# Optimization experiments

Hardware: AMD Instinct MI355X
Metric: run time of the kernel (lower is better)

The kernel has to match this reference:

```python
import jax, jax.numpy as jnp
import numpy as np

D_MODEL = 2048
HQ = 32
HK = 8
DK = D_MODEL // HQ  # 64
G = HQ // HK        # 4
VOCAB = 32000
B, S = 1, 2048


def setup_inputs() -> dict:
    key = jax.random.key(0)
    ks = jax.random.split(key, 7)
    scale = 1.0 / np.sqrt(D_MODEL)
    X = jax.random.randint(ks[0], (B, S), 0, VOCAB, dtype=jnp.int64)
    emb = jax.random.normal(ks[1], (VOCAB, D_MODEL), dtype=jnp.float32)
    Wk = jax.random.normal(ks[2], (HK * DK, D_MODEL), dtype=jnp.float32) * scale
    Wv = jax.random.normal(ks[3], (HK * DK, D_MODEL), dtype=jnp.float32) * scale
    Wq = jax.random.normal(ks[4], (D_MODEL, D_MODEL), dtype=jnp.float32) * scale
    Wo_w = jax.random.normal(ks[5], (D_MODEL, D_MODEL), dtype=jnp.float32) * scale
    Wo_b = jax.random.normal(ks[6], (D_MODEL,), dtype=jnp.float32) * scale
    return {"X": X, "emb": emb, "Wk": Wk, "Wv": Wv, "Wq": Wq, "Wo_w": Wo_w, "Wo_b": Wo_b}


def reference(X, emb, Wk, Wv, Wq, Wo_w, Wo_b):
    e = emb[X]  # [B,S,D]
    b, s, _ = e.shape
    # torch Linear: y = x @ W.T (weights stored [out,in])
    k = (e @ Wk.T).reshape(b, s, HK, DK)            # [B,S,Hk,dk]
    v = (e @ Wv.T).reshape(b, s, HK, DK)            # [B,S,Hk,dk]
    q = (e @ Wq.T).reshape(b, s, HK, G, DK)         # q head index = i*G + g
    # scores: [B,Hk,G,S,S] — same math as expanding KV to Hq heads, no copy
    scores = jnp.einsum('bsigd,btid->bigst', q, k) / jnp.sqrt(jnp.asarray(DK, e.dtype))
    w = jax.nn.softmax(scores, axis=-1)
    ctx = jnp.einsum('bigst,btid->bsigd', w, v).reshape(b, s, D_MODEL)
    return ctx @ Wo_w.T + Wo_b
```

## Files before the change

### kernel.cpp

```cpp
#include <hip/hip_runtime.h>


typedef __bf16 bf16x8 __attribute__((ext_vector_type(8)));
typedef float f32x4 __attribute__((ext_vector_type(4)));
typedef float f32x16 __attribute__((ext_vector_type(16)));
typedef unsigned short ushort8_t __attribute__((ext_vector_type(8)));
typedef unsigned int uint4_t __attribute__((ext_vector_type(4)));

#define DEVI static __device__ __forceinline__

#define QSCALE 0.180336880111112f

DEVI unsigned short f2bf(float f) {
    union { float f; unsigned int u; } c; c.f = f;
    unsigned int u = c.u;
    unsigned int r = (u + 0x7FFFu + ((u >> 16) & 1u)) >> 16;
    return (unsigned short)r;
}

DEVI f32x4 mfma16(bf16x8 a, bf16x8 b, f32x4 c) {
    return __builtin_amdgcn_mfma_f32_16x16x32_bf16(a, b, c, 0, 0, 0);
}
DEVI f32x16 mfma32(bf16x8 a, bf16x8 b, f32x16 c) {
    return __builtin_amdgcn_mfma_f32_32x32x16_bf16(a, b, c, 0, 0, 0);
}
DEVI unsigned cvtpk(float a, float b) {
    unsigned r;
    asm("v_cvt_pk_bf16_f32 %0, %1, %2" : "=v"(r) : "v"(a), "v"(b));
    return r;
}
DEVI void plswap(unsigned& a, unsigned& b) {
    asm("v_permlane32_swap_b32 %0, %1" : "+v"(a), "+v"(b));
}
DEVI void gload16(const unsigned short* g, unsigned short* l) {
    __builtin_amdgcn_global_load_lds(
        (const __attribute__((address_space(1))) void*)g,
        (__attribute__((address_space(3))) void*)l, 16, 0, 0);
}
#define WAIT_VM(n) asm volatile("s_waitcnt vmcnt(" #n ")" ::: "memory")
#define WAIT_LGKM0() asm volatile("s_waitcnt lgkmcnt(0)" ::: "memory")
#define BAR() __builtin_amdgcn_s_barrier()

DEVI void cvt8(const float* src, unsigned short* dst) {
    float4 f0 = *(const float4*)(src);
    float4 f1 = *(const float4*)(src + 4);
    ushort8_t v;
    v[0] = f2bf(f0.x); v[1] = f2bf(f0.y); v[2] = f2bf(f0.z); v[3] = f2bf(f0.w);
    v[4] = f2bf(f1.x); v[5] = f2bf(f1.y); v[6] = f2bf(f1.z); v[7] = f2bf(f1.w);
    *(ushort8_t*)(dst) = v;
}

__global__ __launch_bounds__(256)
void prep_k(const int* __restrict__ X, const float* __restrict__ emb,
            unsigned short* __restrict__ e,
            const float* __restrict__ Wk, unsigned short* __restrict__ Wkb,
            const float* __restrict__ Wv, unsigned short* __restrict__ Wvb,
            const float* __restrict__ Wq, unsigned short* __restrict__ Wqb,
            const float* __restrict__ Wo, unsigned short* __restrict__ Wob) {
    int b = blockIdx.x;
    if (b < 2048) {
        long long row = X[b];
        cvt8(emb + row * 2048 + threadIdx.x * 8, e + (size_t)b * 2048 + threadIdx.x * 8);
        return;
    }
    b -= 2048;
    const float* s; unsigned short* d; int off;
    if (b < 512) { s = Wk; d = Wkb; off = b; }
    else if (b < 1024) { s = Wv; d = Wvb; off = b - 512; }
    else if (b < 3072) { s = Wq; d = Wqb; off = b - 1024; }
    else { s = Wo; d = Wob; off = b - 3072; }
    size_t idx = ((size_t)off * 256 + threadIdx.x) * 8;
    cvt8(s + idx, d + idx);
}

template<int OM0, int OM1, int OM2>
__global__ __launch_bounds__(256)
void gemm_swz_k(const unsigned short* __restrict__ A,
                const unsigned short* __restrict__ W0, const unsigned short* __restrict__ W1,
                const unsigned short* __restrict__ W2,
                void* __restrict__ C0, void* __restrict__ C1, void* __restrict__ C2,
                int t1, int t2, int ldc0, int ldc1, int ldc2,
                const float* __restrict__ bias) {
    __shared__ unsigned short As[2 * 128 * 64];
    __shared__ unsigned short Bs[2 * 128 * 64];
    const int cpx = gridDim.x >> 3;
    int id = blockIdx.x;
    int swz = (id & 7) * cpx + (id >> 3);
    const int bx = swz & 15;
    const int by = swz >> 4;
    const unsigned short* Wp; void* Cp; int ldc, om, nb;
    if (by < t1)      { Wp = W0; Cp = C0; ldc = ldc0; om = OM0; nb = by; }
    else if (by < t2) { Wp = W1; Cp = C1; ldc = ldc1; om = OM1; nb = by - t1; }
    else              { Wp = W2; Cp = C2; ldc = ldc2; om = OM2; nb = by - t2; }
    const int m0 = bx * 128, n0 = nb * 128;
    const int tid = threadIdx.x, lane = tid & 63, w = tid >> 6;
    const int wm = (w >> 1) * 64, wn = (w & 1) * 64;
    const int lr = lane & 15, lg = lane >> 4;
    const int srow = tid >> 3, sj = tid & 7;

    f32x4 acc[4][4];
    #pragma unroll
    for (int i = 0; i < 4; i++)
        #pragma unroll
        for (int j = 0; j < 4; j++) acc[i][j] = {};

    #define G_STAGE(buf, k0)                                                          \
        _Pragma("unroll")                                                             \
        for (int i = 0; i < 4; i++) {                                                 \
            int row = srow + i * 32;                                                  \
            int jj = sj ^ (row & 7);                                                  \
            unsigned short* ad = As + (buf) * 8192 + (w * 64 + i * 256) * 8;          \
            unsigned short* bd = Bs + (buf) * 8192 + (w * 64 + i * 256) * 8;          \
            gload16(A  + (size_t)(m0 + row) * 2048 + (k0) + jj * 8, ad);              \
            gload16(Wp + (size_t)(n0 + row) * 2048 + (k0) + jj * 8, bd);              \
        }

    G_STAGE(0, 0);
    for (int s = 0; s < 32; ++s) {
        const int cur = s & 1;
        if (s < 31) {
            G_STAGE(cur ^ 1, (s + 1) * 64);
            WAIT_VM(8);
        } else {
            WAIT_VM(0);
        }
        BAR();
        const unsigned short* Asb = As + cur * 8192;
        const unsigned short* Bsb = Bs + cur * 8192;
        #pragma unroll
        for (int kk = 0; kk < 2; kk++) {
            bf16x8 af[4], bfr[4];
            #pragma unroll
            for (int mi = 0; mi < 4; mi++) {
                int r = wm + mi * 16 + lr;
                int g = (kk * 4 + lg) ^ (r & 7);
                af[mi] = *(const bf16x8*)(&Asb[r * 64 + g * 8]);
            }
            #pragma unroll
            for (int ni = 0; ni < 4; ni++) {
                int r = wn + ni * 16 + lr;
                int g = (kk * 4 + lg) ^ (r & 7);
                bfr[ni] = *(const bf16x8*)(&Bsb[r * 64 + g * 8]);
            }
            __builtin_amdgcn_s_setprio(1);
            #pragma unroll
            for (int mi = 0; mi < 4; mi++)
                #pragma unroll
                for (int ni = 0; ni < 4; ni++)
                    acc[mi][ni] = mfma16(af[mi], bfr[ni], acc[mi][ni]);
            __builtin_amdgcn_s_setprio(0);
        }
        WAIT_LGKM0();
        BAR();
    }
    #undef G_STAGE

    #pragma unroll
    for (int mi = 0; mi < 4; mi++)
        #pragma unroll
        for (int ni = 0; ni < 4; ni++) {
            int col = n0 + wn + ni * 16 + lr;
            #pragma unroll
            for (int jj = 0; jj < 4; jj++) {
                int rowg = m0 + wm + mi * 16 + lg * 4 + jj;
                float vv = acc[mi][ni][jj];
                if (om == 0) {
                    ((unsigned short*)Cp)[(size_t)rowg * ldc + col] = f2bf(vv);
                } else if (om == 1) {
                    ((float*)Cp)[(size_t)rowg * ldc + col] = vv + bias[col];
                } else if (om == 2) {
                    ((unsigned short*)Cp)[(size_t)col * ldc + rowg] = f2bf(vv);
                } else {
                    ((unsigned short*)Cp)[(size_t)rowg * ldc + col] = f2bf(vv * QSCALE);
                }
            }
        }
}

__global__ __launch_bounds__(256)
void attn2_k(const unsigned short* __restrict__ Qb, const unsigned short* __restrict__ Kb,
             const unsigned short* __restrict__ VbT, unsigned short* __restrict__ Ctx) {
    __shared__ unsigned short Ks[2 * 64 * 64];
    __shared__ unsigned short Vts[2 * 64 * 64];
    int id = blockIdx.x;
    int swz = (id & 7) * 64 + (id >> 3);
    const int hq = swz >> 4;
    const int qt = swz & 15;
    const int ikv = hq >> 2;
    const int tid = threadIdx.x, lane = tid & 63, w = tid >> 6;
    const int l31 = lane & 31, hi = lane >> 5;
    const int qrow = qt * 128 + w * 32 + l31;
    const int srow = tid >> 3, sj = tid & 7;

    bf16x8 qf[4];
    #pragma unroll
    for (int ks = 0; ks < 4; ks++)
        qf[ks] = *(const bf16x8*)(Qb + (size_t)qrow * 2048 + hq * 64 + ks * 16 + hi * 8);

    bf16x8 onesb;
    #pragma unroll
    for (int i = 0; i < 8; i++) onesb[i] = (__bf16)1.0f;

    f32x16 oacc0 = {}, oacc1 = {}, lacc = {};
    float m = -1e30f;

    #define A_STAGE(buf, t0)                                                          \
        _Pragma("unroll")                                                             \
        for (int i = 0; i < 2; i++) {                                                 \
            int row = srow + i * 32;                                                  \
            int jj = sj ^ (row & 7);                                                  \
            unsigned short* kd = Ks + (buf) * 4096 + (w * 64 + i * 256) * 8;          \
            unsigned short* vd = Vts + (buf) * 4096 + (w * 64 + i * 256) * 8;         \
            gload16(Kb + (size_t)((t0) + row) * 512 + ikv * 64 + jj * 8, kd);         \
            gload16(VbT + (size_t)(ikv * 64 + row) * 2048 + (t0) + jj * 8, vd);       \
        }

    A_STAGE(0, 0);
    for (int t = 0; t < 32; ++t) {
        const int cur = t & 1;
        if (t < 31) {
            A_STAGE(cur ^ 1, (t + 1) * 64);
            WAIT_VM(4);
        } else {
            WAIT_VM(0);
        }
        BAR();
        const unsigned short* Ksb = Ks + cur * 4096;
        const unsigned short* Vsb = Vts + cur * 4096;

        f32x16 s0 = {}, s1 = {};
        __builtin_amdgcn_s_setprio(1);
        #pragma unroll
        for (int ks = 0; ks < 4; ks++) {
            int gr = (2 * ks + hi) ^ (l31 & 7);
            bf16x8 kf0 = *(const bf16x8*)(&Ksb[l31 * 64 + gr * 8]);
            bf16x8 kf1 = *(const bf16x8*)(&Ksb[(32 + l31) * 64 + gr * 8]);
            s0 = mfma32(kf0, qf[ks], s0);
            s1 = mfma32(kf1, qf[ks], s1);
        }
        __builtin_amdgcn_s_setprio(0);

        float a0 = fmaxf(fmaxf(s0[0],  s0[1]),  s0[2]);
        float a1 = fmaxf(fmaxf(s0[3],  s0[4]),  s0[5]);
        float a2 = fmaxf(fmaxf(s0[6],  s0[7]),  s0[8]);
        float a3 = fmaxf(fmaxf(s0[9],  s0[10]), s0[11]);
        float a4 = fmaxf(fmaxf(s0[12], s0[13]), s0[14]);
        float b0 = fmaxf(fmaxf(s1[0],  s1[1]),  s1[2]);
        float b1 = fmaxf(fmaxf(s1[3],  s1[4]),  s1[5]);
        float b2 = fmaxf(fmaxf(s1[6],  s1[7]),  s1[8]);
        float b3 = fmaxf(fmaxf(s1[9],  s1[10]), s1[11]);
        float b4 = fmaxf(fmaxf(s1[12], s1[13]), s1[14]);
        float c0 = fmaxf(s0[15], s1[15]);
        float d0 = fmaxf(fmaxf(a0, a1), a2);
        float d1 = fmaxf(fmaxf(a3, a4), b0);
        float d2 = fmaxf(fmaxf(b1, b2), b3);
        float d3 = fmaxf(fmaxf(b4, c0), d0);
        float pmax = fmaxf(fmaxf(d1, d2), d3);
        pmax = fmaxf(pmax, __shfl_xor(pmax, 32, 64));

        if (!__all(pmax <= m + 8.0f)) {
            float mnew = fmaxf(m, pmax);
            float sc = exp2f(m - mnew);
            m = mnew;
            #pragma unroll
            for (int r = 0; r < 16; r++) {
                const int qp = (r & 3) + 8 * (r >> 2);
                float scv = __shfl(sc, qp + 4 * hi, 64);
                oacc0[r] *= scv;
                oacc1[r] *= scv;
                lacc[r] *= scv;
            }
        }

        #pragma unroll
        for (int r = 0; r < 16; r++) {
            s0[r] = exp2f(s0[r] - m);
            s1[r] = exp2f(s1[r] - m);
        }

        uint4_t pw[4];
        #pragma unroll
        for (int c = 0; c < 2; c++) {
            unsigned a   = cvtpk(s0[8 * c + 0], s0[8 * c + 1]);
            unsigned bb  = cvtpk(s0[8 * c + 2], s0[8 * c + 3]);
            unsigned cc2 = cvtpk(s0[8 * c + 4], s0[8 * c + 5]);
            unsigned dd  = cvtpk(s0[8 * c + 6], s0[8 * c + 7]);
            plswap(a, cc2); plswap(bb, dd);
            pw[c][0] = a; pw[c][1] = bb; pw[c][2] = cc2; pw[c][3] = dd;
        }
        #pragma unroll
        for (int c = 0; c < 2; c++) {
            unsigned a   = cvtpk(s1[8 * c + 0], s1[8 * c + 1]);
            unsigned bb  = cvtpk(s1[8 * c + 2], s1[8 * c + 3]);
            unsigned cc2 = cvtpk(s1[8 * c + 4], s1[8 * c + 5]);
            unsigned dd  = cvtpk(s1[8 * c + 6], s1[8 * c + 7]);
            plswap(a, cc2); plswap(bb, dd);
            pw[2 + c][0] = a; pw[2 + c][1] = bb; pw[2 + c][2] = cc2; pw[2 + c][3] = dd;
        }

        __builtin_amdgcn_s_setprio(1);
        #pragma unroll
        for (int ks = 0; ks < 4; ks++) {
            bf16x8 pa = __builtin_bit_cast(bf16x8, pw[ks]);
            int gr = (2 * ks + hi) ^ (l31 & 7);
            bf16x8 vf0 = *(const bf16x8*)(&Vsb[l31 * 64 + gr * 8]);
            bf16x8 vf1 = *(const bf16x8*)(&Vsb[(32 + l31) * 64 + gr * 8]);
            oacc0 = mfma32(pa, vf0, oacc0);
            oacc1 = mfma32(pa, vf1, oacc1);
            lacc  = mfma32(pa, onesb, lacc);
        }
        __builtin_amdgcn_s_setprio(0);
        WAIT_LGKM0();
        BAR();
    }
    #undef A_STAGE

    #pragma unroll
    for (int r = 0; r < 16; r++) {
        float lv = 1.0f / lacc[r];
        int row = qt * 128 + w * 32 + (r & 3) + 8 * (r >> 2) + 4 * hi;
        Ctx[(size_t)row * 2048 + hq * 64 + l31]      = f2bf(oacc0[r] * lv);
        Ctx[(size_t)row * 2048 + hq * 64 + 32 + l31] = f2bf(oacc1[r] * lv);
    }
}

extern "C" void kernel_launch(void* const* d_in, const int* in_sizes, int n_in,
                              void* d_out, int out_size, void* d_ws, size_t ws_size,
                              hipStream_t stream) {
    (void)in_sizes; (void)n_in; (void)out_size; (void)ws_size;
    const int*   X   = (const int*)d_in[0];
    const float* emb = (const float*)d_in[1];
    const float* Wk  = (const float*)d_in[2];
    const float* Wv  = (const float*)d_in[3];
    const float* Wq  = (const float*)d_in[4];
    const float* Wo  = (const float*)d_in[5];
    const float* Wb  = (const float*)d_in[6];

    unsigned short* e   = (unsigned short*)d_ws;
    unsigned short* Kb  = e   + (size_t)2048 * 2048;
    unsigned short* VbT = Kb  + (size_t)2048 * 512;
    unsigned short* Qb  = VbT + (size_t)512 * 2048;
    unsigned short* Ctx = Qb  + (size_t)2048 * 2048;
    unsigned short* Wkb = Ctx + (size_t)2048 * 2048;
    unsigned short* Wvb = Wkb + (size_t)512 * 2048;
    unsigned short* Wqb = Wvb + (size_t)512 * 2048;
    unsigned short* Wob = Wqb + (size_t)2048 * 2048;

    prep_k<<<dim3(2048 + 5120), dim3(256), 0, stream>>>(X, emb, e, Wk, Wkb, Wv, Wvb,
                                                        Wq, Wqb, Wo, Wob);
    gemm_swz_k<3, 0, 2><<<dim3(384), dim3(256), 0, stream>>>(
        e, Wqb, Wkb, Wvb, (void*)Qb, (void*)Kb, (void*)VbT,
        16, 20, 2048, 512, 2048, nullptr);
    attn2_k<<<dim3(512), dim3(256), 0, stream>>>(Qb, Kb, VbT, Ctx);
    gemm_swz_k<1, 1, 1><<<dim3(256), dim3(256), 0, stream>>>(
        Ctx, Wob, Wob, Wob, d_out, d_out, d_out,
        16, 32, 2048, 2048, 2048, Wb);
}
```

Measured before the change: 162.9 us.

## Load K/V fragments directly from global memory into registers in attention

```diff
diff --git a/kernel.cpp b/kernel.cpp
--- a/kernel.cpp
+++ b/kernel.cpp
@@ -178,19 +178,16 @@
 }
 
 __global__ __launch_bounds__(256)
-void attn2_k(const unsigned short* __restrict__ Qb, const unsigned short* __restrict__ Kb,
+void attn3_k(const unsigned short* __restrict__ Qb, const unsigned short* __restrict__ Kb,
              const unsigned short* __restrict__ VbT, unsigned short* __restrict__ Ctx) {
-    __shared__ unsigned short Ks[2 * 64 * 64];
-    __shared__ unsigned short Vts[2 * 64 * 64];
     int id = blockIdx.x;
     int swz = (id & 7) * 64 + (id >> 3);
     const int hq = swz >> 4;
     const int qt = swz & 15;
     const int ikv = hq >> 2;
-    const int tid = threadIdx.x, lane = tid & 63, w = tid >> 6;
+    const int lane = threadIdx.x & 63, w = threadIdx.x >> 6;
     const int l31 = lane & 31, hi = lane >> 5;
     const int qrow = qt * 128 + w * 32 + l31;
-    const int srow = tid >> 3, sj = tid & 7;
 
     bf16x8 qf[4];
     #pragma unroll
@@ -201,42 +198,33 @@
     #pragma unroll
     for (int i = 0; i < 8; i++) onesb[i] = (__bf16)1.0f;
 
+    const unsigned short* Kp0 = Kb + (size_t)l31 * 512 + ikv * 64 + hi * 8;
+    const unsigned short* Kp1 = Kp0 + (size_t)32 * 512;
+    const unsigned short* Vp0 = VbT + (size_t)(ikv * 64 + l31) * 2048 + hi * 8;
+    const unsigned short* Vp1 = Vp0 + (size_t)32 * 2048;
+
     f32x16 oacc0 = {}, oacc1 = {}, lacc = {};
     float m = -1e30f;
 
-    #define A_STAGE(buf, t0)                                                          \
-        _Pragma("unroll")                                                             \
-        for (int i = 0; i < 2; i++) {                                                 \
-            int row = srow + i * 32;                                                  \
-            int jj = sj ^ (row & 7);                                                  \
-            unsigned short* kd = Ks + (buf) * 4096 + (w * 64 + i * 256) * 8;          \
-            unsigned short* vd = Vts + (buf) * 4096 + (w * 64 + i * 256) * 8;         \
-            gload16(Kb + (size_t)((t0) + row) * 512 + ikv * 64 + jj * 8, kd);         \
-            gload16(VbT + (size_t)(ikv * 64 + row) * 2048 + (t0) + jj * 8, vd);       \
-        }
-
-    A_STAGE(0, 0);
-    for (int t = 0; t < 32; ++t) {
-        const int cur = t & 1;
-        if (t < 31) {
-            A_STAGE(cur ^ 1, (t + 1) * 64);
-            WAIT_VM(4);
-        } else {
-            WAIT_VM(0);
-        }
-        BAR();
-        const unsigned short* Ksb = Ks + cur * 4096;
-        const unsigned short* Vsb = Vts + cur * 4096;
+    for (int t0 = 0; t0 < 2048; t0 += 64) {
+        bf16x8 kf0[4], kf1[4], vf0[4], vf1[4];
+        #pragma unroll
+        for (int ks = 0; ks < 4; ks++) {
+            kf0[ks] = *(const bf16x8*)(Kp0 + (size_t)t0 * 512 + ks * 16);
+            kf1[ks] = *(const bf16x8*)(Kp1 + (size_t)t0 * 512 + ks * 16);
+        }
+        #pragma unroll
+        for (int ks = 0; ks < 4; ks++) {
+            vf0[ks] = *(const bf16x8*)(Vp0 + t0 + ks * 16);
+            vf1[ks] = *(const bf16x8*)(Vp1 + t0 + ks * 16);
+        }
 
         f32x16 s0 = {}, s1 = {};
         __builtin_amdgcn_s_setprio(1);
         #pragma unroll
         for (int ks = 0; ks < 4; ks++) {
-            int gr = (2 * ks + hi) ^ (l31 & 7);
-            bf16x8 kf0 = *(const bf16x8*)(&Ksb[l31 * 64 + gr * 8]);
-            bf16x8 kf1 = *(const bf16x8*)(&Ksb[(32 + l31) * 64 + gr * 8]);
-            s0 = mfma32(kf0, qf[ks], s0);
-            s1 = mfma32(kf1, qf[ks], s1);
+            s0 = mfma32(kf0[ks], qf[ks], s0);
+            s1 = mfma32(kf1[ks], qf[ks], s1);
         }
         __builtin_amdgcn_s_setprio(0);
 
@@ -302,18 +290,12 @@
         #pragma unroll
         for (int ks = 0; ks < 4; ks++) {
             bf16x8 pa = __builtin_bit_cast(bf16x8, pw[ks]);
-            int gr = (2 * ks + hi) ^ (l31 & 7);
-            bf16x8 vf0 = *(const bf16x8*)(&Vsb[l31 * 64 + gr * 8]);
-            bf16x8 vf1 = *(const bf16x8*)(&Vsb[(32 + l31) * 64 + gr * 8]);
-            oacc0 = mfma32(pa, vf0, oacc0);
-            oacc1 = mfma32(pa, vf1, oacc1);
+            oacc0 = mfma32(pa, vf0[ks], oacc0);
+            oacc1 = mfma32(pa, vf1[ks], oacc1);
             lacc  = mfma32(pa, onesb, lacc);
         }
         __builtin_amdgcn_s_setprio(0);
-        WAIT_LGKM0();
-        BAR();
     }
-    #undef A_STAGE
 
     #pragma unroll
     for (int r = 0; r < 16; r++) {
@@ -351,7 +333,7 @@
     gemm_swz_k<3, 0, 2><<<dim3(384), dim3(256), 0, stream>>>(
         e, Wqb, Wkb, Wvb, (void*)Qb, (void*)Kb, (void*)VbT,
         16, 20, 2048, 512, 2048, nullptr);
-    attn2_k<<<dim3(512), dim3(256), 0, stream>>>(Qb, Kb, VbT, Ctx);
+    attn3_k<<<dim3(512), dim3(256), 0, stream>>>(Qb, Kb, VbT, Ctx);
     gemm_swz_k<1, 1, 1><<<dim3(256), dim3(256), 0, stream>>>(
         Ctx, Wob, Wob, Wob, d_out, d_out, d_out,
         16, 32, 2048, 2048, 2048, Wb);
```

New measurement: 219.8 us. 1.35x slower.

## Split attention KV range in two and merge partials with combine kernel

Applied to the files above, without the earlier changes.

```diff
diff --git a/kernel.cpp b/kernel.cpp
--- a/kernel.cpp
+++ b/kernel.cpp
@@ -178,12 +178,15 @@
 }
 
 __global__ __launch_bounds__(256)
-void attn2_k(const unsigned short* __restrict__ Qb, const unsigned short* __restrict__ Kb,
-             const unsigned short* __restrict__ VbT, unsigned short* __restrict__ Ctx) {
+void attn4_k(const unsigned short* __restrict__ Qb, const unsigned short* __restrict__ Kb,
+             const unsigned short* __restrict__ VbT,
+             float* __restrict__ Op, float* __restrict__ Mb, float* __restrict__ Lb) {
     __shared__ unsigned short Ks[2 * 64 * 64];
     __shared__ unsigned short Vts[2 * 64 * 64];
     int id = blockIdx.x;
-    int swz = (id & 7) * 64 + (id >> 3);
+    const int sp = id >> 9;
+    int orig = id & 511;
+    int swz = (orig & 7) * 64 + (orig >> 3);
     const int hq = swz >> 4;
     const int qt = swz & 15;
     const int ikv = hq >> 2;
@@ -191,6 +194,7 @@
     const int l31 = lane & 31, hi = lane >> 5;
     const int qrow = qt * 128 + w * 32 + l31;
     const int srow = tid >> 3, sj = tid & 7;
+    const int tbase = sp * 1024;
 
     bf16x8 qf[4];
     #pragma unroll
@@ -215,11 +219,11 @@
             gload16(VbT + (size_t)(ikv * 64 + row) * 2048 + (t0) + jj * 8, vd);       \
         }
 
-    A_STAGE(0, 0);
-    for (int t = 0; t < 32; ++t) {
+    A_STAGE(0, tbase);
+    for (int t = 0; t < 16; ++t) {
         const int cur = t & 1;
-        if (t < 31) {
-            A_STAGE(cur ^ 1, (t + 1) * 64);
+        if (t < 15) {
+            A_STAGE(cur ^ 1, tbase + (t + 1) * 64);
             WAIT_VM(4);
         } else {
             WAIT_VM(0);
@@ -315,13 +319,48 @@
     }
     #undef A_STAGE
 
+    float* Ops = Op + (size_t)sp * 2048 * 2048;
     #pragma unroll
     for (int r = 0; r < 16; r++) {
-        float lv = 1.0f / lacc[r];
-        int row = qt * 128 + w * 32 + (r & 3) + 8 * (r >> 2) + 4 * hi;
-        Ctx[(size_t)row * 2048 + hq * 64 + l31]      = f2bf(oacc0[r] * lv);
-        Ctx[(size_t)row * 2048 + hq * 64 + 32 + l31] = f2bf(oacc1[r] * lv);
+        int crow = (r & 3) + 8 * (r >> 2) + 4 * hi;
+        int row = qt * 128 + w * 32 + crow;
+        Ops[(size_t)row * 2048 + hq * 64 + l31]      = oacc0[r];
+        Ops[(size_t)row * 2048 + hq * 64 + 32 + l31] = oacc1[r];
+        if (l31 == 0)
+            Lb[sp * 65536 + hq * 2048 + row] = lacc[r];
     }
+    if (hi == 0)
+        Mb[sp * 65536 + hq * 2048 + qt * 128 + w * 32 + l31] = m;
+}
+
+__global__ __launch_bounds__(256)
+void comb_k(const float* __restrict__ Op, const float* __restrict__ Mb,
+            const float* __restrict__ Lb, unsigned short* __restrict__ Ctx) {
+    const int row = blockIdx.x, t = threadIdx.x;
+    const int h = t >> 3;
+    float m1 = Mb[h * 2048 + row], m2 = Mb[65536 + h * 2048 + row];
+    float l1 = Lb[h * 2048 + row], l2 = Lb[65536 + h * 2048 + row];
+    float M = fmaxf(m1, m2);
+    float w1 = exp2f(m1 - M), w2 = exp2f(m2 - M);
+    float inv = 1.0f / (l1 * w1 + l2 * w2);
+    w1 *= inv; w2 *= inv;
+    size_t base = (size_t)row * 2048 + t * 8;
+    const float* p1 = Op + base;
+    const float* p2 = Op + (size_t)2048 * 2048 + base;
+    float4 a0 = *(const float4*)(p1);
+    float4 a1 = *(const float4*)(p1 + 4);
+    float4 b0 = *(const float4*)(p2);
+    float4 b1 = *(const float4*)(p2 + 4);
+    ushort8_t v;
+    v[0] = f2bf(a0.x * w1 + b0.x * w2);
+    v[1] = f2bf(a0.y * w1 + b0.y * w2);
+    v[2] = f2bf(a0.z * w1 + b0.z * w2);
+    v[3] = f2bf(a0.w * w1 + b0.w * w2);
+    v[4] = f2bf(a1.x * w1 + b1.x * w2);
+    v[5] = f2bf(a1.y * w1 + b1.y * w2);
+    v[6] = f2bf(a1.z * w1 + b1.z * w2);
+    v[7] = f2bf(a1.w * w1 + b1.w * w2);
+    *(ushort8_t*)(Ctx + base) = v;
 }
 
 extern "C" void kernel_launch(void* const* d_in, const int* in_sizes, int n_in,
@@ -345,13 +384,17 @@
     unsigned short* Wvb = Wkb + (size_t)512 * 2048;
     unsigned short* Wqb = Wvb + (size_t)512 * 2048;
     unsigned short* Wob = Wqb + (size_t)2048 * 2048;
+    float* Op = (float*)(Wob + (size_t)2048 * 2048);
+    float* Mb = Op + (size_t)2 * 2048 * 2048;
+    float* Lb = Mb + (size_t)2 * 65536;
 
     prep_k<<<dim3(2048 + 5120), dim3(256), 0, stream>>>(X, emb, e, Wk, Wkb, Wv, Wvb,
                                                         Wq, Wqb, Wo, Wob);
     gemm_swz_k<3, 0, 2><<<dim3(384), dim3(256), 0, stream>>>(
         e, Wqb, Wkb, Wvb, (void*)Qb, (void*)Kb, (void*)VbT,
         16, 20, 2048, 512, 2048, nullptr);
-    attn2_k<<<dim3(512), dim3(256), 0, stream>>>(Qb, Kb, VbT, Ctx);
+    attn4_k<<<dim3(1024), dim3(256), 0, stream>>>(Qb, Kb, VbT, Op, Mb, Lb);
+    comb_k<<<dim3(2048), dim3(256), 0, stream>>>(Op, Mb, Lb, Ctx);
     gemm_swz_k<1, 1, 1><<<dim3(256), dim3(256), 0, stream>>>(
         Ctx, Wob, Wob, Wob, d_out, d_out, d_out,
         16, 32, 2048, 2048, 2048, Wb);
```

Measured after the change: 176.6 us. 1.08x slower.
